# Kernel tuning notes

Hardware: AMD Instinct MI355X
Metric: run time of the kernel (lower is better)

The kernel has to match this reference:

```python
import jax, jax.numpy as jnp
import numpy as np
from jax import lax

DIM = 192
HEADS = 8
NBLK = 4  # self.N


def _dwconv(x, w, groups):
    # x: (B,C,H,W), w: (O, C//groups, k, k), padding = k//2 ('SAME')
    return lax.conv_general_dilated(
        x, w, window_strides=(1, 1), padding='SAME',
        feature_group_count=groups,
        dimension_numbers=('NCHW', 'OIHW', 'NCHW'))


def _conv1x1(x, w, b):
    # w: (O, C), b: (O,)
    return jnp.einsum('bchw,oc->bohw', x, w) + b[None, :, None, None]


def _mdc(x, w1, w2, w3, w4):
    g = DIM // 4
    x1 = _dwconv(x, w1, g)
    x2 = _dwconv(x, w2, g)
    x3 = _dwconv(x, w3, g)
    x4 = _dwconv(x, w4, g)
    out = jnp.concatenate([x1, x2, x3, x4], axis=1)
    return jax.nn.sigmoid(x) * out


def _to_heads(x, b, h, w):
    # 'b (head c) (h1 hs) (w1 ws) -> b head (c h1 w1) (hs ws)', h1=w1=NBLK
    c = DIM // HEADS
    hs, ws = h // NBLK, w // NBLK
    x = x.reshape(b, HEADS, c, NBLK, hs, NBLK, ws)
    x = x.transpose(0, 1, 2, 3, 5, 4, 6)  # b head c h1 w1 hs ws
    return x.reshape(b, HEADS, c * NBLK * NBLK, hs * ws)


def _from_heads(x, b, h, w):
    c = DIM // HEADS
    hs, ws = h // NBLK, w // NBLK
    x = x.reshape(b, HEADS, c, NBLK, NBLK, hs, ws)
    x = x.transpose(0, 1, 2, 3, 5, 4, 6)  # b head c h1 hs w1 ws
    return x.reshape(b, HEADS * c, h, w)


def setup_inputs() -> dict:
    key = jax.random.key(0)
    ks = jax.random.split(key, 16)
    B, H, W = 2, 256, 256
    g = DIM // 4
    s = 0.05
    return {
        'xu': jax.random.normal(ks[0], (B, DIM, H, W), jnp.float32),
        'xd': jax.random.normal(ks[1], (B, DIM, H, W), jnp.float32),
        'temperature': jnp.ones((HEADS, 1, 1), jnp.float32),
        'q1_w': jax.random.normal(ks[2], (DIM, DIM), jnp.float32) * s,
        'q1_b': jnp.zeros((DIM,), jnp.float32),
        'k1_w': jax.random.normal(ks[3], (DIM, DIM), jnp.float32) * s,
        'k1_b': jnp.zeros((DIM,), jnp.float32),
        'v1_w': jax.random.normal(ks[4], (DIM, DIM), jnp.float32) * s,
        'v1_b': jnp.zeros((DIM,), jnp.float32),
        'mdcq_w': jax.random.normal(ks[5], (DIM, 1, 3, 3), jnp.float32) * s,
        'mdck_w': jax.random.normal(ks[6], (DIM, 1, 3, 3), jnp.float32) * s,
        'mdc1_w': jax.random.normal(ks[7], (g, 4, 3, 3), jnp.float32) * s,
        'mdc2_w': jax.random.normal(ks[8], (g, 4, 5, 5), jnp.float32) * s,
        'mdc3_w': jax.random.normal(ks[9], (g, 4, 7, 7), jnp.float32) * s,
        'mdc4_w': jax.random.normal(ks[10], (g, 4, 9, 9), jnp.float32) * s,
        'proj_w': jax.random.normal(ks[11], (DIM, DIM), jnp.float32) * s,
        'proj_b': jnp.zeros((DIM,), jnp.float32),
    }


def reference(xu, xd, temperature, q1_w, q1_b, k1_w, k1_b, v1_w, v1_b,
              mdcq_w, mdck_w, mdc1_w, mdc2_w, mdc3_w, mdc4_w, proj_w, proj_b):
    b, c0, h11, w11 = xu.shape
    h_pad = (NBLK - h11 % NBLK) % NBLK
    w_pad = (NBLK - w11 % NBLK) % NBLK
    if h_pad or w_pad:
        pad = ((0, 0), (0, 0), (0, h_pad), (0, w_pad))
        xu_1 = jnp.pad(xu, pad, mode='reflect')
        xd_1 = jnp.pad(xd, pad, mode='reflect')
    else:
        xu_1, xd_1 = xu, xd
    h, w = xu_1.shape[2], xu_1.shape[3]

    q1 = _dwconv(_conv1x1(xu_1, q1_w, q1_b), mdcq_w, DIM)
    k1 = _dwconv(_conv1x1(xd_1, k1_w, k1_b), mdck_w, DIM)
    v1 = _mdc(_conv1x1(xd_1, v1_w, v1_b), mdc1_w, mdc2_w, mdc3_w, mdc4_w)

    q = _to_heads(q1, b, h, w)
    k = _to_heads(k1, b, h, w)
    v = _to_heads(v1, b, h, w)

    # L2-normalize over tokens (last dim); torch F.normalize eps=1e-12
    q = q / jnp.maximum(jnp.linalg.norm(q, axis=-1, keepdims=True), 1e-12)
    k = k / jnp.maximum(jnp.linalg.norm(k, axis=-1, keepdims=True), 1e-12)

    attn = jnp.einsum('bhct,bhdt->bhcd', q, k) * temperature[None]
    attn = jax.nn.softmax(attn, axis=-1)
    out = jnp.einsum('bhcd,bhdt->bhct', attn, v)

    out = _from_heads(out, b, h, w)
    out = _conv1x1(out, proj_w, proj_b)
    return out[:, :, :h11, :w11]
```

## Files before the change

kernel.cpp:

```cpp
#include <hip/hip_runtime.h>
#include <math.h>

#define CDIM 192
#define HW 65536

typedef __attribute__((ext_vector_type(8))) short short8;
typedef __attribute__((ext_vector_type(4))) float f32x4;

__device__ __forceinline__ ushort f2bf(float f) {
  uint u = __float_as_uint(f);
  uint r = (u + 0x7fffu + ((u >> 16) & 1u)) >> 16;
  return (ushort)r;
}
__device__ __forceinline__ float bf2f(ushort u) {
  return __uint_as_float(((uint)u) << 16);
}

__device__ __forceinline__ size_t rowbase(int b, int head, int r, int hs) {
  int c = r >> 4, h1 = (r >> 2) & 3, w1 = r & 3;
  return ((size_t)(b * CDIM + head * 24 + c) << 16) +
         (size_t)((h1 << 6) + hs) * 256 + (w1 << 6);
}

__global__ __launch_bounds__(256) void cast_f32_nhwc_kernel(
    const float* __restrict__ in, ushort* __restrict__ out) {
  __shared__ ushort T[64][200];
  const int p0 = blockIdx.x << 6, b = blockIdx.y;
  const int tid = threadIdx.x;
#pragma unroll
  for (int it = 0; it < 12; ++it) {
    int idx = (it << 8) + tid;
    int c = idx >> 4, p4 = (idx & 15) << 2;
    float4 v = *(const float4*)&in[((size_t)(b * CDIM + c) << 16) + p0 + p4];
    T[p4 + 0][c] = f2bf(v.x);
    T[p4 + 1][c] = f2bf(v.y);
    T[p4 + 2][c] = f2bf(v.z);
    T[p4 + 3][c] = f2bf(v.w);
  }
  __syncthreads();
#pragma unroll
  for (int it = 0; it < 6; ++it) {
    int idx = (it << 8) + tid;
    int p = idx / 24, c8 = (idx % 24) << 3;
    *(uint4*)&out[((size_t)(b * HW + p0 + p)) * CDIM + c8] =
        *(uint4*)&T[p][c8];
  }
}

__global__ __launch_bounds__(256) void cast_bf16_nhwc_kernel(
    const ushort* __restrict__ in, ushort* __restrict__ out) {
  __shared__ ushort T[64][200];
  const int p0 = blockIdx.x << 6, b = blockIdx.y;
  const int tid = threadIdx.x;
#pragma unroll
  for (int it = 0; it < 6; ++it) {
    int idx = (it << 8) + tid;
    int c = idx >> 3, p8 = (idx & 7) << 3;
    uint4 v = *(const uint4*)&in[((size_t)(b * CDIM + c) << 16) + p0 + p8];
    const ushort* pv = (const ushort*)&v;
#pragma unroll
    for (int q = 0; q < 8; ++q) T[p8 + q][c] = pv[q];
  }
  __syncthreads();
#pragma unroll
  for (int it = 0; it < 6; ++it) {
    int idx = (it << 8) + tid;
    int p = idx / 24, c8 = (idx % 24) << 3;
    *(uint4*)&out[((size_t)(b * HW + p0 + p)) * CDIM + c8] =
        *(uint4*)&T[p][c8];
  }
}

template <int OUTF32>
__global__ __launch_bounds__(256) void conv_mfma_kernel(
    const ushort* __restrict__ Xt, const float* __restrict__ w,
    const float* __restrict__ bias, void* __restrict__ outv) {
  __shared__ ushort WL[64][200];
  __shared__ ushort XL[256][72];
  const int p0 = blockIdx.x << 8;
  const int o0 = blockIdx.y << 6;
  const int b  = blockIdx.z;
  const int tid = threadIdx.x;
  const int wave = tid >> 6, lane = tid & 63;
  const int lr = lane & 15, lk = lane >> 4;
#pragma unroll
  for (int it = 0; it < 12; ++it) {
    int idx = (it << 8) + tid;
    int o = idx / 48, c4 = (idx % 48) << 2;
    float4 v = *(const float4*)&w[(o0 + o) * CDIM + c4];
    ushort4 u = make_ushort4(f2bf(v.x), f2bf(v.y), f2bf(v.z), f2bf(v.w));
    *(ushort4*)&WL[o][c4] = u;
  }
  f32x4 acc[4][4] = {};
  const size_t xbase = ((size_t)(b * HW + p0)) * CDIM;
  for (int kt = 0; kt < 3; ++kt) {
    __syncthreads();
#pragma unroll
    for (int it = 0; it < 8; ++it) {
      int idx = (it << 8) + tid;
      int p = idx >> 3, c8 = (idx & 7) << 3;
      *(uint4*)&XL[p][c8] =
          *(const uint4*)&Xt[xbase + (size_t)p * CDIM + kt * 64 + c8];
    }
    __syncthreads();
#pragma unroll
    for (int kk = 0; kk < 2; ++kk) {
      short8 aF[4], bF[4];
#pragma unroll
      for (int m = 0; m < 4; ++m)
        aF[m] = *(const short8*)&WL[(m << 4) + lr][kt * 64 + (kk << 5) + (lk << 3)];
#pragma unroll
      for (int n = 0; n < 4; ++n)
        bF[n] = *(const short8*)&XL[(wave << 6) + (n << 4) + lr][(kk << 5) + (lk << 3)];
#pragma unroll
      for (int m = 0; m < 4; ++m)
#pragma unroll
        for (int n = 0; n < 4; ++n)
          acc[m][n] =
              __builtin_amdgcn_mfma_f32_16x16x32_bf16(aF[m], bF[n], acc[m][n], 0, 0, 0);
    }
  }
#pragma unroll
  for (int m = 0; m < 4; ++m)
#pragma unroll
    for (int reg = 0; reg < 4; ++reg) {
      int i = o0 + (m << 4) + (lk << 2) + reg;
      float bo = bias[i];
      size_t ob = ((size_t)(b * CDIM + i) << 16) + p0 + (wave << 6) + lr;
#pragma unroll
      for (int n = 0; n < 4; ++n) {
        float v = acc[m][n][reg] + bo;
        if (OUTF32)
          ((float*)outv)[ob + (n << 4)] = v;
        else
          ((ushort*)outv)[ob + (n << 4)] = f2bf(v);
      }
    }
}

__global__ __launch_bounds__(256) void dw3x3_bf16_kernel(
    const ushort* __restrict__ in, const float* __restrict__ wdw,
    ushort* __restrict__ outb) {
  size_t idx = ((size_t)blockIdx.x << 8) + threadIdx.x;
  int x0 = (int)(idx & 63) << 2;
  int y  = (int)((idx >> 6) & 255);
  int bc = (int)(idx >> 14);
  int ch = bc % CDIM, b = bc / CDIM;
  const ushort* ip = in + ((size_t)bc << 16);
  const float* wp = wdw + ch * 9;
  float wv[9];
#pragma unroll
  for (int k = 0; k < 9; ++k) wv[k] = wp[k];
  float r[3][6];
#pragma unroll
  for (int dy = 0; dy < 3; ++dy) {
    int yy = y + dy - 1;
    bool yok = (yy >= 0) && (yy < 256);
#pragma unroll
    for (int dx = 0; dx < 6; ++dx) {
      int xx = x0 + dx - 1;
      bool ok = yok && (xx >= 0) && (xx < 256);
      r[dy][dx] = ok ? bf2f(ip[(size_t)yy * 256 + xx]) : 0.f;
    }
  }
  float o_[4];
#pragma unroll
  for (int j = 0; j < 4; ++j) {
    float a = 0.f;
#pragma unroll
    for (int dy = 0; dy < 3; ++dy)
#pragma unroll
      for (int dx = 0; dx < 3; ++dx)
        a = fmaf(r[dy][j + dx], wv[dy * 3 + dx], a);
    o_[j] = a;
  }
  int head = ch / 24, c = ch % 24;
  int h1 = y >> 6, hs = y & 63, w1 = x0 >> 6, ws0 = x0 & 63;
  int bh = (b << 3) + head;
  int rr = (c << 4) + (h1 << 2) + w1;
  *(ushort4*)&outb[((size_t)(bh * 384 + rr) << 12) + (hs << 6) + ws0] =
      make_ushort4(f2bf(o_[0]), f2bf(o_[1]), f2bf(o_[2]), f2bf(o_[3]));
}

__global__ __launch_bounds__(256) void mdc_fused_kernel(
    const ushort* __restrict__ in, const float* __restrict__ w3,
    const float* __restrict__ w5, const float* __restrict__ w7,
    const float* __restrict__ w9, ushort* __restrict__ out) {
  __shared__ float s[4][40][40];
  const int bz = blockIdx.z;
  const int b = bz / 48, g = bz % 48;
  const int x0 = blockIdx.x << 5, y0 = blockIdx.y << 5;
  const ushort* inb = in + (((size_t)b * CDIM + 4 * g) << 16);
  for (int idx = threadIdx.x; idx < 1600; idx += 256) {
    int rowid = idx / 10, c = idx % 10;
    int i = rowid / 40, yy = rowid % 40;
    int y = y0 + yy - 4;
    int xs = x0 + (c << 2) - 4;
    float4 v = make_float4(0.f, 0.f, 0.f, 0.f);
    if (y >= 0 && y < 256 && xs >= 0 && xs < 256) {
      ushort4 u = *(const ushort4*)&inb[((size_t)i << 16) + (size_t)y * 256 + xs];
      v = make_float4(bf2f(u.x), bf2f(u.y), bf2f(u.z), bf2f(u.w));
    }
    *(float4*)&s[i][yy][c << 2] = v;
  }
  __syncthreads();
  const int tx = threadIdx.x & 7;
  const int ty = threadIdx.x >> 3;
  float a3[4] = {}, a5[4] = {}, a7[4] = {}, a9[4] = {};
#pragma unroll 1
  for (int i = 0; i < 4; ++i) {
    const float* w9p = w9 + (g * 4 + i) * 81;
    const float* w7p = w7 + (g * 4 + i) * 49;
    const float* w5p = w5 + (g * 4 + i) * 25;
    const float* w3p = w3 + (g * 4 + i) * 9;
#pragma unroll
    for (int ky = 0; ky < 9; ++ky) {
      float row[12];
      *(float4*)&row[0] = *(const float4*)&s[i][ty + ky][(tx << 2)];
      *(float4*)&row[4] = *(const float4*)&s[i][ty + ky][(tx << 2) + 4];
      *(float4*)&row[8] = *(const float4*)&s[i][ty + ky][(tx << 2) + 8];
#pragma unroll
      for (int kx = 0; kx < 9; ++kx) {
        float w = w9p[ky * 9 + kx];
#pragma unroll
        for (int j = 0; j < 4; ++j) a9[j] = fmaf(row[j + kx], w, a9[j]);
      }
      if (ky >= 1 && ky <= 7) {
#pragma unroll
        for (int kx = 0; kx < 7; ++kx) {
          float w = w7p[(ky - 1) * 7 + kx];
#pragma unroll
          for (int j = 0; j < 4; ++j) a7[j] = fmaf(row[j + kx + 1], w, a7[j]);
        }
      }
      if (ky >= 2 && ky <= 6) {
#pragma unroll
        for (int kx = 0; kx < 5; ++kx) {
          float w = w5p[(ky - 2) * 5 + kx];
#pragma unroll
          for (int j = 0; j < 4; ++j) a5[j] = fmaf(row[j + kx + 2], w, a5[j]);
        }
      }
      if (ky >= 3 && ky <= 5) {
#pragma unroll
        for (int kx = 0; kx < 3; ++kx) {
          float w = w3p[(ky - 3) * 3 + kx];
#pragma unroll
          for (int j = 0; j < 4; ++j) a3[j] = fmaf(row[j + kx + 3], w, a3[j]);
        }
      }
    }
  }
  const int yo = y0 + ty, xo = x0 + (tx << 2);
#pragma unroll
  for (int sel = 0; sel < 4; ++sel) {
    const float* ap = (sel == 0) ? a3 : (sel == 1) ? a5 : (sel == 2) ? a7 : a9;
    int oc = sel * 48 + g;
    size_t off = (((size_t)b * CDIM + oc) << 16) + (size_t)yo * 256 + xo;
    ushort4 u = *(const ushort4*)&in[off];
    float s0 = 1.f / (1.f + expf(-bf2f(u.x)));
    float s1 = 1.f / (1.f + expf(-bf2f(u.y)));
    float s2 = 1.f / (1.f + expf(-bf2f(u.z)));
    float s3 = 1.f / (1.f + expf(-bf2f(u.w)));
    *(ushort4*)&out[off] = make_ushort4(f2bf(s0 * ap[0]), f2bf(s1 * ap[1]),
                                        f2bf(s2 * ap[2]), f2bf(s3 * ap[3]));
  }
}

__global__ __launch_bounds__(256) void norm_bf16_kernel(
    const ushort* __restrict__ Qb, const ushort* __restrict__ Kb,
    float* __restrict__ nrm) {
  const int which = blockIdx.y;
  const int id = (blockIdx.x << 2) + (threadIdx.x >> 6);
  const int lane = threadIdx.x & 63;
  const ushort* row = (which ? Kb : Qb) + ((size_t)id << 12);
  float s = 0.f;
#pragma unroll
  for (int e = 0; e < 8; ++e) {
    uint4 u = *(const uint4*)&row[(e << 9) + (lane << 3)];
    uint us[4] = {u.x, u.y, u.z, u.w};
#pragma unroll
    for (int q = 0; q < 4; ++q) {
      float lo = __uint_as_float(us[q] << 16);
      float hi = __uint_as_float(us[q] & 0xffff0000u);
      s = fmaf(lo, lo, s);
      s = fmaf(hi, hi, s);
    }
  }
#pragma unroll
  for (int o = 32; o; o >>= 1) s += __shfl_down(s, o, 64);
  if (lane == 0) nrm[which * 6144 + id] = 1.f / fmaxf(sqrtf(s), 1e-12f);
}

__global__ __launch_bounds__(256) void qk_mfma_kernel(
    const ushort* __restrict__ Qb, const ushort* __restrict__ Kb,
    float* __restrict__ part) {
  __shared__ ushort as_[128][72];
  __shared__ ushort bs_[128][72];
  const int bz = blockIdx.z, bh = bz >> 2, ks = bz & 3;
  const int i0 = blockIdx.y << 7, j0 = blockIdx.x << 7;
  const int tid = threadIdx.x;
  const int wave = tid >> 6, lane = tid & 63;
  const int wr = wave >> 1, wc = wave & 1;
  const int lr = lane & 15, lk = lane >> 4;
  const size_t qbase = ((size_t)(bh * 384 + i0) << 12) + (ks << 10);
  const size_t kbase = ((size_t)(bh * 384 + j0) << 12) + (ks << 10);
  f32x4 acc[4][4] = {};
  for (int kt = 0; kt < 16; ++kt) {
#pragma unroll
    for (int e = 0; e < 4; ++e) {
      int chunk = (e << 8) + tid;
      int row = chunk >> 3, c8 = (chunk & 7) << 3;
      *(uint4*)&as_[row][c8] =
          *(const uint4*)&Qb[qbase + ((size_t)row << 12) + (kt << 6) + c8];
      *(uint4*)&bs_[row][c8] =
          *(const uint4*)&Kb[kbase + ((size_t)row << 12) + (kt << 6) + c8];
    }
    __syncthreads();
#pragma unroll
    for (int kk = 0; kk < 2; ++kk) {
      short8 aF[4], bF[4];
#pragma unroll
      for (int m = 0; m < 4; ++m)
        aF[m] = *(const short8*)&as_[(wr << 6) + (m << 4) + lr][(kk << 5) + (lk << 3)];
#pragma unroll
      for (int n = 0; n < 4; ++n)
        bF[n] = *(const short8*)&bs_[(wc << 6) + (n << 4) + lr][(kk << 5) + (lk << 3)];
#pragma unroll
      for (int m = 0; m < 4; ++m)
#pragma unroll
        for (int n = 0; n < 4; ++n)
          acc[m][n] =
              __builtin_amdgcn_mfma_f32_16x16x32_bf16(aF[m], bF[n], acc[m][n], 0, 0, 0);
    }
    __syncthreads();
  }
  float* pbase = part + (size_t)(ks * 16 + bh) * 384 * 384;
#pragma unroll
  for (int m = 0; m < 4; ++m)
#pragma unroll
    for (int reg = 0; reg < 4; ++reg) {
      int i = i0 + (wr << 6) + (m << 4) + (lk << 2) + reg;
#pragma unroll
      for (int n = 0; n < 4; ++n) {
        int j = j0 + (wc << 6) + (n << 4) + lr;
        pbase[(size_t)i * 384 + j] = acc[m][n][reg];
      }
    }
}

__global__ __launch_bounds__(384) void softmax_kernel(
    const float* __restrict__ part, const float* __restrict__ nrm,
    const float* __restrict__ temp, ushort* __restrict__ Pb) {
  const int row = blockIdx.x;
  const int bh = row / 384;
  const int head = bh & 7;
  const int tid = threadIdx.x;
  const size_t off = (size_t)row * 384 + tid;
  float s = part[off] + part[off + 2359296] + part[off + 4718592] +
            part[off + 7077888];
  float v = s * temp[head] * nrm[row] * nrm[6144 + bh * 384 + tid];
  __shared__ float red[6];
  float m = v;
#pragma unroll
  for (int o = 32; o; o >>= 1) m = fmaxf(m, __shfl_down(m, o, 64));
  if ((tid & 63) == 0) red[tid >> 6] = m;
  __syncthreads();
  float bm = fmaxf(fmaxf(fmaxf(red[0], red[1]), fmaxf(red[2], red[3])),
                   fmaxf(red[4], red[5]));
  __syncthreads();
  float e = expf(v - bm);
  float ss = e;
#pragma unroll
  for (int o = 32; o; o >>= 1) ss += __shfl_down(ss, o, 64);
  if ((tid & 63) == 0) red[tid >> 6] = ss;
  __syncthreads();
  float bs = red[0] + red[1] + red[2] + red[3] + red[4] + red[5];
  Pb[off] = f2bf(e / bs);
}

__global__ __launch_bounds__(256) void pack_v_kernel(
    const ushort* __restrict__ v1, ushort* __restrict__ Vb) {
  __shared__ ushort st[384][72];
  const int hs = blockIdx.x, bh = blockIdx.y;
  const int b = bh >> 3, head = bh & 7;
  const int tid = threadIdx.x;
#pragma unroll
  for (int e = 0; e < 12; ++e) {
    int idx = (e << 8) + tid;
    int r = idx >> 3, w8 = (idx & 7) << 3;
    *(uint4*)&st[r][w8] = *(const uint4*)&v1[rowbase(b, head, r, hs) + w8];
  }
  __syncthreads();
  const size_t vb0 = ((size_t)bh * 4096 + (hs << 6)) * 384;
#pragma unroll
  for (int e = 0; e < 12; ++e) {
    int chunk = (e << 8) + tid;
    int trow = chunk & 63, c8 = (chunk >> 6) << 3;
    ushort tmp[8];
#pragma unroll
    for (int q = 0; q < 8; ++q) tmp[q] = st[c8 + q][trow];
    *(uint4*)&Vb[vb0 + (size_t)trow * 384 + c8] = *(uint4*)tmp;
  }
}

__global__ __launch_bounds__(256) void pv_mfma_kernel(
    const ushort* __restrict__ Pb, const ushort* __restrict__ Vb,
    ushort* __restrict__ outh) {
  __shared__ ushort as_[128][72];
  __shared__ ushort bs_[128][72];
  const int bh = blockIdx.z, b = bh >> 3, head = bh & 7;
  const int i0 = blockIdx.y << 7, t0 = blockIdx.x << 7;
  const int tid = threadIdx.x;
  const int wave = tid >> 6, lane = tid & 63;
  const int wr = wave >> 1, wc = wave & 1;
  const int lr = lane & 15, lk = lane >> 4;
  const size_t pbase = (size_t)(bh * 384 + i0) * 384;
  const size_t vbase = ((size_t)bh * 4096 + t0) * 384;
  f32x4 acc[4][4] = {};
  for (int kt = 0; kt < 6; ++kt) {
#pragma unroll
    for (int e = 0; e < 4; ++e) {
      int chunk = (e << 8) + tid;
      int row = chunk >> 3, c8 = (chunk & 7) << 3;
      *(uint4*)&as_[row][c8] =
          *(const uint4*)&Pb[pbase + (size_t)row * 384 + (kt << 6) + c8];
      *(uint4*)&bs_[row][c8] =
          *(const uint4*)&Vb[vbase + (size_t)row * 384 + (kt << 6) + c8];
    }
    __syncthreads();
#pragma unroll
    for (int kk = 0; kk < 2; ++kk) {
      short8 aF[4], bF[4];
#pragma unroll
      for (int m = 0; m < 4; ++m)
        aF[m] = *(const short8*)&as_[(wr << 6) + (m << 4) + lr][(kk << 5) + (lk << 3)];
#pragma unroll
      for (int n = 0; n < 4; ++n)
        bF[n] = *(const short8*)&bs_[(wc << 6) + (n << 4) + lr][(kk << 5) + (lk << 3)];
#pragma unroll
      for (int m = 0; m < 4; ++m)
#pragma unroll
        for (int n = 0; n < 4; ++n)
          acc[m][n] =
              __builtin_amdgcn_mfma_f32_16x16x32_bf16(aF[m], bF[n], acc[m][n], 0, 0, 0);
    }
    __syncthreads();
  }
#pragma unroll
  for (int m = 0; m < 4; ++m)
#pragma unroll
    for (int reg = 0; reg < 4; ++reg) {
      int i = i0 + (wr << 6) + (m << 4) + (lk << 2) + reg;
#pragma unroll
      for (int n = 0; n < 4; ++n) {
        int t = t0 + (wc << 6) + (n << 4) + lr;
        outh[rowbase(b, head, i, t >> 6) + (t & 63)] = f2bf(acc[m][n][reg]);
      }
    }
}

extern "C" void kernel_launch(void* const* d_in, const int* in_sizes, int n_in,
                              void* d_out, int out_size, void* d_ws,
                              size_t ws_size, hipStream_t stream) {
  const float* xu     = (const float*)d_in[0];
  const float* xd     = (const float*)d_in[1];
  const float* temp   = (const float*)d_in[2];
  const float* q1_w   = (const float*)d_in[3];
  const float* q1_b   = (const float*)d_in[4];
  const float* k1_w   = (const float*)d_in[5];
  const float* k1_b   = (const float*)d_in[6];
  const float* v1_w   = (const float*)d_in[7];
  const float* v1_b   = (const float*)d_in[8];
  const float* mdcq_w = (const float*)d_in[9];
  const float* mdck_w = (const float*)d_in[10];
  const float* mdc1_w = (const float*)d_in[11];
  const float* mdc2_w = (const float*)d_in[12];
  const float* mdc3_w = (const float*)d_in[13];
  const float* mdc4_w = (const float*)d_in[14];
  const float* proj_w = (const float*)d_in[15];
  const float* proj_b = (const float*)d_in[16];
  float* out = (float*)d_out;

  const size_t SZ = (size_t)2 * CDIM * HW * 2;
  char* W = (char*)d_ws;
  ushort* A0 = (ushort*)(W + 0 * SZ);
  ushort* A1 = (ushort*)(W + 1 * SZ);
  ushort* A2 = (ushort*)(W + 2 * SZ);
  ushort* A3 = (ushort*)(W + 3 * SZ);
  ushort* A4 = (ushort*)(W + 4 * SZ);
  float*  PART = (float*)(W + 5 * SZ);
  ushort* Pb   = (ushort*)(W + 5 * SZ + 37748736);
  float*  NRM  = (float*)(W + 5 * SZ + 37748736 + 4718592);

  dim3 b256(256);
  dim3 gcast(1024, 2);
  dim3 gconv(256, 3, 2);

  cast_f32_nhwc_kernel<<<gcast, b256, 0, stream>>>(xu, A0);
  cast_f32_nhwc_kernel<<<gcast, b256, 0, stream>>>(xd, A1);
  conv_mfma_kernel<0><<<gconv, b256, 0, stream>>>(A0, q1_w, q1_b, A2);
  dw3x3_bf16_kernel<<<24576, b256, 0, stream>>>(A2, mdcq_w, A3);
  conv_mfma_kernel<0><<<gconv, b256, 0, stream>>>(A1, k1_w, k1_b, A0);
  dw3x3_bf16_kernel<<<24576, b256, 0, stream>>>(A0, mdck_w, A4);
  norm_bf16_kernel<<<dim3(1536, 2), b256, 0, stream>>>(A3, A4, NRM);
  qk_mfma_kernel<<<dim3(3, 3, 64), b256, 0, stream>>>(A3, A4, PART);
  softmax_kernel<<<6144, dim3(384), 0, stream>>>(PART, NRM, temp, Pb);
  conv_mfma_kernel<0><<<gconv, b256, 0, stream>>>(A1, v1_w, v1_b, A2);
  mdc_fused_kernel<<<dim3(8, 8, 96), b256, 0, stream>>>(
      A2, mdc1_w, mdc2_w, mdc3_w, mdc4_w, A3);
  pack_v_kernel<<<dim3(64, 16), b256, 0, stream>>>(A3, A4);
  pv_mfma_kernel<<<dim3(32, 3, 16), b256, 0, stream>>>(Pb, A4, A1);
  cast_bf16_nhwc_kernel<<<gcast, b256, 0, stream>>>(A1, A2);
  conv_mfma_kernel<1><<<gconv, b256, 0, stream>>>(A2, proj_w, proj_b, out);
}
```

Measured before the change: 637.4 us.

## Retile MDC fused conv to column-wise 8-row register blocking with taller tiles

The multi-kernel depthwise conv kernel now processes 32x64 output tiles instead of 32x32. Each thread computes 8 vertically adjacent outputs from a 16-element column held in registers, sweeping kx in the outer loop. This raises register reuse per shared-memory load and halves the halo overhead per tile. The trade-offs are more registers, scalar rather than vector shared and global accesses, and half as many blocks in the grid.

```diff
diff --git a/kernel.cpp b/kernel.cpp
--- a/kernel.cpp
+++ b/kernel.cpp
@@ -186,14 +186,14 @@
     const ushort* __restrict__ in, const float* __restrict__ w3,
     const float* __restrict__ w5, const float* __restrict__ w7,
     const float* __restrict__ w9, ushort* __restrict__ out) {
-  __shared__ float s[4][40][40];
+  __shared__ float s[4][72][40];
   const int bz = blockIdx.z;
   const int b = bz / 48, g = bz % 48;
-  const int x0 = blockIdx.x << 5, y0 = blockIdx.y << 5;
+  const int x0 = blockIdx.x << 5, y0 = blockIdx.y << 6;
   const ushort* inb = in + (((size_t)b * CDIM + 4 * g) << 16);
-  for (int idx = threadIdx.x; idx < 1600; idx += 256) {
+  for (int idx = threadIdx.x; idx < 2880; idx += 256) {
     int rowid = idx / 10, c = idx % 10;
-    int i = rowid / 40, yy = rowid % 40;
+    int i = rowid / 72, yy = rowid % 72;
     int y = y0 + yy - 4;
     int xs = x0 + (c << 2) - 4;
     float4 v = make_float4(0.f, 0.f, 0.f, 0.f);
@@ -204,9 +204,9 @@
     *(float4*)&s[i][yy][c << 2] = v;
   }
   __syncthreads();
-  const int tx = threadIdx.x & 7;
-  const int ty = threadIdx.x >> 3;
-  float a3[4] = {}, a5[4] = {}, a7[4] = {}, a9[4] = {};
+  const int x = threadIdx.x & 31;
+  const int ys = (threadIdx.x >> 5) << 3;
+  float a3[8] = {}, a5[8] = {}, a7[8] = {}, a9[8] = {};
 #pragma unroll 1
   for (int i = 0; i < 4; ++i) {
     const float* w9p = w9 + (g * 4 + i) * 81;
@@ -214,56 +214,55 @@
     const float* w5p = w5 + (g * 4 + i) * 25;
     const float* w3p = w3 + (g * 4 + i) * 9;
 #pragma unroll
-    for (int ky = 0; ky < 9; ++ky) {
-      float row[12];
-      *(float4*)&row[0] = *(const float4*)&s[i][ty + ky][(tx << 2)];
-      *(float4*)&row[4] = *(const float4*)&s[i][ty + ky][(tx << 2) + 4];
-      *(float4*)&row[8] = *(const float4*)&s[i][ty + ky][(tx << 2) + 8];
-#pragma unroll
-      for (int kx = 0; kx < 9; ++kx) {
+    for (int kx = 0; kx < 9; ++kx) {
+      float col[16];
+#pragma unroll
+      for (int yy = 0; yy < 16; ++yy)
+        col[yy] = s[i][ys + yy][x + kx];
+#pragma unroll
+      for (int ky = 0; ky < 9; ++ky) {
         float w = w9p[ky * 9 + kx];
 #pragma unroll
-        for (int j = 0; j < 4; ++j) a9[j] = fmaf(row[j + kx], w, a9[j]);
-      }
-      if (ky >= 1 && ky <= 7) {
-#pragma unroll
-        for (int kx = 0; kx < 7; ++kx) {
-          float w = w7p[(ky - 1) * 7 + kx];
-#pragma unroll
-          for (int j = 0; j < 4; ++j) a7[j] = fmaf(row[j + kx + 1], w, a7[j]);
+        for (int y = 0; y < 8; ++y) a9[y] = fmaf(col[y + ky], w, a9[y]);
+      }
+      if (kx >= 1 && kx <= 7) {
+#pragma unroll
+        for (int ky = 0; ky < 7; ++ky) {
+          float w = w7p[ky * 7 + kx - 1];
+#pragma unroll
+          for (int y = 0; y < 8; ++y) a7[y] = fmaf(col[y + ky + 1], w, a7[y]);
         }
       }
-      if (ky >= 2 && ky <= 6) {
-#pragma unroll
-        for (int kx = 0; kx < 5; ++kx) {
-          float w = w5p[(ky - 2) * 5 + kx];
-#pragma unroll
-          for (int j = 0; j < 4; ++j) a5[j] = fmaf(row[j + kx + 2], w, a5[j]);
+      if (kx >= 2 && kx <= 6) {
+#pragma unroll
+        for (int ky = 0; ky < 5; ++ky) {
+          float w = w5p[ky * 5 + kx - 2];
+#pragma unroll
+          for (int y = 0; y < 8; ++y) a5[y] = fmaf(col[y + ky + 2], w, a5[y]);
         }
       }
-      if (ky >= 3 && ky <= 5) {
-#pragma unroll
-        for (int kx = 0; kx < 3; ++kx) {
-          float w = w3p[(ky - 3) * 3 + kx];
-#pragma unroll
-          for (int j = 0; j < 4; ++j) a3[j] = fmaf(row[j + kx + 3], w, a3[j]);
+      if (kx >= 3 && kx <= 5) {
+#pragma unroll
+        for (int ky = 0; ky < 3; ++ky) {
+          float w = w3p[ky * 3 + kx - 3];
+#pragma unroll
+          for (int y = 0; y < 8; ++y) a3[y] = fmaf(col[y + ky + 3], w, a3[y]);
         }
       }
     }
   }
-  const int yo = y0 + ty, xo = x0 + (tx << 2);
+  const int xo = x0 + x;
 #pragma unroll
   for (int sel = 0; sel < 4; ++sel) {
     const float* ap = (sel == 0) ? a3 : (sel == 1) ? a5 : (sel == 2) ? a7 : a9;
     int oc = sel * 48 + g;
-    size_t off = (((size_t)b * CDIM + oc) << 16) + (size_t)yo * 256 + xo;
-    ushort4 u = *(const ushort4*)&in[off];
-    float s0 = 1.f / (1.f + expf(-bf2f(u.x)));
-    float s1 = 1.f / (1.f + expf(-bf2f(u.y)));
-    float s2 = 1.f / (1.f + expf(-bf2f(u.z)));
-    float s3 = 1.f / (1.f + expf(-bf2f(u.w)));
-    *(ushort4*)&out[off] = make_ushort4(f2bf(s0 * ap[0]), f2bf(s1 * ap[1]),
-                                        f2bf(s2 * ap[2]), f2bf(s3 * ap[3]));
+    size_t base = (((size_t)b * CDIM + oc) << 16) + (size_t)(y0 + ys) * 256 + xo;
+#pragma unroll
+    for (int y = 0; y < 8; ++y) {
+      ushort u = in[base + (size_t)y * 256];
+      float sg = 1.f / (1.f + expf(-bf2f(u)));
+      out[base + (size_t)y * 256] = f2bf(sg * ap[y]);
+    }
   }
 }
 
@@ -507,7 +506,7 @@
   qk_mfma_kernel<<<dim3(3, 3, 64), b256, 0, stream>>>(A3, A4, PART);
   softmax_kernel<<<6144, dim3(384), 0, stream>>>(PART, NRM, temp, Pb);
   conv_mfma_kernel<0><<<gconv, b256, 0, stream>>>(A1, v1_w, v1_b, A2);
-  mdc_fused_kernel<<<dim3(8, 8, 96), b256, 0, stream>>>(
+  mdc_fused_kernel<<<dim3(8, 4, 96), b256, 0, stream>>>(
       A2, mdc1_w, mdc2_w, mdc3_w, mdc4_w, A3);
   pack_v_kernel<<<dim3(64, 16), b256, 0, stream>>>(A3, A4);
   pv_mfma_kernel<<<dim3(32, 3, 16), b256, 0, stream>>>(Pb, A4, A1);
```

Result: slower. 684.1 us (+7.3%).

## Fuse L2 norm into depthwise conv via atomics, merge casts, use fast math

Applied to the files above, without the earlier changes.

Removes the separate norm kernel by having the depthwise 3x3 conv accumulate sum of squares of its bf16-rounded outputs. Each 16-lane group reduces with shuffles and then does an atomicAdd into a zeroed buffer, and softmax converts the sums to inverse norms. The two f32-to-bf16 NHWC casts are merged into one launch using blockIdx.z. The mdc kernel prefetches its sigmoid inputs before the main loop and uses fast exp/rcp, and softmax uses fast exp/rcp. This saves one full read pass over Q and K and a launch, at the cost of atomic traffic, an extra zeroing kernel, and slightly less accurate math.

```diff
diff --git a/kernel.cpp b/kernel.cpp
--- a/kernel.cpp
+++ b/kernel.cpp
@@ -22,10 +22,17 @@
          (size_t)((h1 << 6) + hs) * 256 + (w1 << 6);
 }
 
+__global__ __launch_bounds__(256) void zero_nrm_kernel(float* __restrict__ p) {
+  p[(blockIdx.x << 8) + threadIdx.x] = 0.f;
+}
+
 __global__ __launch_bounds__(256) void cast_f32_nhwc_kernel(
-    const float* __restrict__ in, ushort* __restrict__ out) {
+    const float* __restrict__ in0, const float* __restrict__ in1,
+    ushort* __restrict__ out0, ushort* __restrict__ out1) {
   __shared__ ushort T[64][200];
   const int p0 = blockIdx.x << 6, b = blockIdx.y;
+  const float* in = blockIdx.z ? in1 : in0;
+  ushort* out = blockIdx.z ? out1 : out0;
   const int tid = threadIdx.x;
 #pragma unroll
   for (int it = 0; it < 12; ++it) {
@@ -140,7 +147,7 @@
 
 __global__ __launch_bounds__(256) void dw3x3_bf16_kernel(
     const ushort* __restrict__ in, const float* __restrict__ wdw,
-    ushort* __restrict__ outb) {
+    ushort* __restrict__ outb, float* __restrict__ nrms) {
   size_t idx = ((size_t)blockIdx.x << 8) + threadIdx.x;
   int x0 = (int)(idx & 63) << 2;
   int y  = (int)((idx >> 6) & 255);
@@ -164,6 +171,7 @@
     }
   }
   float o_[4];
+  float ss = 0.f;
 #pragma unroll
   for (int j = 0; j < 4; ++j) {
     float a = 0.f;
@@ -173,6 +181,8 @@
       for (int dx = 0; dx < 3; ++dx)
         a = fmaf(r[dy][j + dx], wv[dy * 3 + dx], a);
     o_[j] = a;
+    float q = bf2f(f2bf(a));
+    ss = fmaf(q, q, ss);
   }
   int head = ch / 24, c = ch % 24;
   int h1 = y >> 6, hs = y & 63, w1 = x0 >> 6, ws0 = x0 & 63;
@@ -180,6 +190,10 @@
   int rr = (c << 4) + (h1 << 2) + w1;
   *(ushort4*)&outb[((size_t)(bh * 384 + rr) << 12) + (hs << 6) + ws0] =
       make_ushort4(f2bf(o_[0]), f2bf(o_[1]), f2bf(o_[2]), f2bf(o_[3]));
+  const int lane = threadIdx.x & 63;
+#pragma unroll
+  for (int off = 8; off; off >>= 1) ss += __shfl_xor(ss, off, 64);
+  if ((lane & 15) == 0) atomicAdd(&nrms[bh * 384 + rr], ss);
 }
 
 __global__ __launch_bounds__(256) void mdc_fused_kernel(
@@ -191,6 +205,16 @@
   const int b = bz / 48, g = bz % 48;
   const int x0 = blockIdx.x << 5, y0 = blockIdx.y << 5;
   const ushort* inb = in + (((size_t)b * CDIM + 4 * g) << 16);
+  const int tx = threadIdx.x & 7;
+  const int ty = threadIdx.x >> 3;
+  const int yo = y0 + ty, xo = x0 + (tx << 2);
+  ushort4 upre[4];
+#pragma unroll
+  for (int sel = 0; sel < 4; ++sel) {
+    int oc = sel * 48 + g;
+    upre[sel] = *(const ushort4*)&in[(((size_t)b * CDIM + oc) << 16) +
+                                     (size_t)yo * 256 + xo];
+  }
   for (int idx = threadIdx.x; idx < 1600; idx += 256) {
     int rowid = idx / 10, c = idx % 10;
     int i = rowid / 40, yy = rowid % 40;
@@ -204,8 +228,6 @@
     *(float4*)&s[i][yy][c << 2] = v;
   }
   __syncthreads();
-  const int tx = threadIdx.x & 7;
-  const int ty = threadIdx.x >> 3;
   float a3[4] = {}, a5[4] = {}, a7[4] = {}, a9[4] = {};
 #pragma unroll 1
   for (int i = 0; i < 4; ++i) {
@@ -251,45 +273,19 @@
       }
     }
   }
-  const int yo = y0 + ty, xo = x0 + (tx << 2);
 #pragma unroll
   for (int sel = 0; sel < 4; ++sel) {
     const float* ap = (sel == 0) ? a3 : (sel == 1) ? a5 : (sel == 2) ? a7 : a9;
     int oc = sel * 48 + g;
     size_t off = (((size_t)b * CDIM + oc) << 16) + (size_t)yo * 256 + xo;
-    ushort4 u = *(const ushort4*)&in[off];
-    float s0 = 1.f / (1.f + expf(-bf2f(u.x)));
-    float s1 = 1.f / (1.f + expf(-bf2f(u.y)));
-    float s2 = 1.f / (1.f + expf(-bf2f(u.z)));
-    float s3 = 1.f / (1.f + expf(-bf2f(u.w)));
+    ushort4 u = upre[sel];
+    float s0 = __builtin_amdgcn_rcpf(1.f + __expf(-bf2f(u.x)));
+    float s1 = __builtin_amdgcn_rcpf(1.f + __expf(-bf2f(u.y)));
+    float s2 = __builtin_amdgcn_rcpf(1.f + __expf(-bf2f(u.z)));
+    float s3 = __builtin_amdgcn_rcpf(1.f + __expf(-bf2f(u.w)));
     *(ushort4*)&out[off] = make_ushort4(f2bf(s0 * ap[0]), f2bf(s1 * ap[1]),
                                         f2bf(s2 * ap[2]), f2bf(s3 * ap[3]));
   }
-}
-
-__global__ __launch_bounds__(256) void norm_bf16_kernel(
-    const ushort* __restrict__ Qb, const ushort* __restrict__ Kb,
-    float* __restrict__ nrm) {
-  const int which = blockIdx.y;
-  const int id = (blockIdx.x << 2) + (threadIdx.x >> 6);
-  const int lane = threadIdx.x & 63;
-  const ushort* row = (which ? Kb : Qb) + ((size_t)id << 12);
-  float s = 0.f;
-#pragma unroll
-  for (int e = 0; e < 8; ++e) {
-    uint4 u = *(const uint4*)&row[(e << 9) + (lane << 3)];
-    uint us[4] = {u.x, u.y, u.z, u.w};
-#pragma unroll
-    for (int q = 0; q < 4; ++q) {
-      float lo = __uint_as_float(us[q] << 16);
-      float hi = __uint_as_float(us[q] & 0xffff0000u);
-      s = fmaf(lo, lo, s);
-      s = fmaf(hi, hi, s);
-    }
-  }
-#pragma unroll
-  for (int o = 32; o; o >>= 1) s += __shfl_down(s, o, 64);
-  if (lane == 0) nrm[which * 6144 + id] = 1.f / fmaxf(sqrtf(s), 1e-12f);
 }
 
 __global__ __launch_bounds__(256) void qk_mfma_kernel(
@@ -350,7 +346,7 @@
 }
 
 __global__ __launch_bounds__(384) void softmax_kernel(
-    const float* __restrict__ part, const float* __restrict__ nrm,
+    const float* __restrict__ part, const float* __restrict__ nrms,
     const float* __restrict__ temp, ushort* __restrict__ Pb) {
   const int row = blockIdx.x;
   const int bh = row / 384;
@@ -359,7 +355,9 @@
   const size_t off = (size_t)row * 384 + tid;
   float s = part[off] + part[off + 2359296] + part[off + 4718592] +
             part[off + 7077888];
-  float v = s * temp[head] * nrm[row] * nrm[6144 + bh * 384 + tid];
+  float iq = 1.f / fmaxf(sqrtf(nrms[row]), 1e-12f);
+  float ik = 1.f / fmaxf(sqrtf(nrms[6144 + bh * 384 + tid]), 1e-12f);
+  float v = s * temp[head] * iq * ik;
   __shared__ float red[6];
   float m = v;
 #pragma unroll
@@ -369,14 +367,14 @@
   float bm = fmaxf(fmaxf(fmaxf(red[0], red[1]), fmaxf(red[2], red[3])),
                    fmaxf(red[4], red[5]));
   __syncthreads();
-  float e = expf(v - bm);
+  float e = __expf(v - bm);
   float ss = e;
 #pragma unroll
   for (int o = 32; o; o >>= 1) ss += __shfl_down(ss, o, 64);
   if ((tid & 63) == 0) red[tid >> 6] = ss;
   __syncthreads();
   float bs = red[0] + red[1] + red[2] + red[3] + red[4] + red[5];
-  Pb[off] = f2bf(e / bs);
+  Pb[off] = f2bf(e * __builtin_amdgcn_rcpf(bs));
 }
 
 __global__ __launch_bounds__(256) void pack_v_kernel(
@@ -494,16 +492,15 @@
   float*  NRM  = (float*)(W + 5 * SZ + 37748736 + 4718592);
 
   dim3 b256(256);
-  dim3 gcast(1024, 2);
+  dim3 gcast(1024, 2, 2);
   dim3 gconv(256, 3, 2);
 
-  cast_f32_nhwc_kernel<<<gcast, b256, 0, stream>>>(xu, A0);
-  cast_f32_nhwc_kernel<<<gcast, b256, 0, stream>>>(xd, A1);
+  zero_nrm_kernel<<<48, b256, 0, stream>>>(NRM);
+  cast_f32_nhwc_kernel<<<gcast, b256, 0, stream>>>(xu, xd, A0, A1);
   conv_mfma_kernel<0><<<gconv, b256, 0, stream>>>(A0, q1_w, q1_b, A2);
-  dw3x3_bf16_kernel<<<24576, b256, 0, stream>>>(A2, mdcq_w, A3);
+  dw3x3_bf16_kernel<<<24576, b256, 0, stream>>>(A2, mdcq_w, A3, NRM);
   conv_mfma_kernel<0><<<gconv, b256, 0, stream>>>(A1, k1_w, k1_b, A0);
-  dw3x3_bf16_kernel<<<24576, b256, 0, stream>>>(A0, mdck_w, A4);
-  norm_bf16_kernel<<<dim3(1536, 2), b256, 0, stream>>>(A3, A4, NRM);
+  dw3x3_bf16_kernel<<<24576, b256, 0, stream>>>(A0, mdck_w, A4, NRM + 6144);
   qk_mfma_kernel<<<dim3(3, 3, 64), b256, 0, stream>>>(A3, A4, PART);
   softmax_kernel<<<6144, dim3(384), 0, stream>>>(PART, NRM, temp, Pb);
   conv_mfma_kernel<0><<<gconv, b256, 0, stream>>>(A1, v1_w, v1_b, A2);
@@ -511,6 +508,6 @@
       A2, mdc1_w, mdc2_w, mdc3_w, mdc4_w, A3);
   pack_v_kernel<<<dim3(64, 16), b256, 0, stream>>>(A3, A4);
   pv_mfma_kernel<<<dim3(32, 3, 16), b256, 0, stream>>>(Pb, A4, A1);
-  cast_bf16_nhwc_kernel<<<gcast, b256, 0, stream>>>(A1, A2);
+  cast_bf16_nhwc_kernel<<<dim3(1024, 2), b256, 0, stream>>>(A1, A2);
   conv_mfma_kernel<1><<<gconv, b256, 0, stream>>>(A2, proj_w, proj_b, out);
 }
```

After: 675.2 us. 1.06x slower.
